# Kernel optimization log

Hardware: AMD Instinct MI355X
Metric: run time of the kernel (lower is better)

The kernel has to match this reference:

```python
import jax, jax.numpy as jnp
import numpy as np

MIN_SCALE = 0.2
MAX_SCALE = 1.0
RESIDUAL_WEIGHT = 0.7


def _conv(x, w, b, pad):
    # x: [B,Cin,H,W], w: [Cout,Cin,k,k]
    y = jax.lax.conv_general_dilated(
        x, w, window_strides=(1, 1), padding=[(pad, pad), (pad, pad)],
        dimension_numbers=("NCHW", "OIHW", "NCHW"))
    return y + b[None, :, None, None]


def setup_inputs() -> dict:
    key = jax.random.key(0)
    ks = jax.random.split(key, 12)
    B, C, H, W = 16, 64, 256, 256
    hidden = C // 2  # max(1, in_channels // 2)
    s = lambda fan_in: 1.0 / np.sqrt(fan_in)
    return {
        "x": jax.random.normal(ks[0], (B, C, H, W), jnp.float32),
        # per-kernel spatial attention convs (2 -> 1 channels)
        "w3": jax.random.normal(ks[1], (1, 2, 3, 3), jnp.float32) * s(2 * 9),
        "b3": jnp.zeros((1,), jnp.float32),
        "w5": jax.random.normal(ks[2], (1, 2, 5, 5), jnp.float32) * s(2 * 25),
        "b5": jnp.zeros((1,), jnp.float32),
        # fusion conv (len(kernel_sizes)=2 -> 1 channels, 1x1)
        "wf": jax.random.normal(ks[3], (1, 2, 1, 1), jnp.float32) * s(2),
        "bf": jnp.zeros((1,), jnp.float32),
        # channel_reduction: C -> 1, 1x1
        "wr": jax.random.normal(ks[4], (1, C, 1, 1), jnp.float32) * s(C),
        "br": jnp.zeros((1,), jnp.float32),
        # channel_attention MLP: 1 -> hidden -> C (1x1 convs)
        "wc1": jax.random.normal(ks[5], (hidden, 1, 1, 1), jnp.float32),
        "bc1": jnp.zeros((hidden,), jnp.float32),
        "wc2": jax.random.normal(ks[6], (C, hidden, 1, 1), jnp.float32) * s(hidden),
        "bc2": jnp.zeros((C,), jnp.float32),
    }


def reference(x, w3, b3, w5, b5, wf, bf, wr, br, wc1, bc1, wc2, bc2):
    # channel-pooled descriptor, shared across scales: [B,2,H,W]
    x_cat = jnp.concatenate(
        [jnp.mean(x, axis=1, keepdims=True), jnp.max(x, axis=1, keepdims=True)],
        axis=1)
    a3 = jax.nn.sigmoid(_conv(x_cat, w3, b3, 1))  # [B,1,H,W]
    a5 = jax.nn.sigmoid(_conv(x_cat, w5, b5, 2))  # [B,1,H,W]
    fused = _conv(jnp.concatenate([a3, a5], axis=1), wf, bf, 0)  # [B,1,H,W]
    # dropout is identity at inference
    fused = MIN_SCALE + (MAX_SCALE - MIN_SCALE) * fused
    spatial = x * fused  # [B,C,H,W]
    # channel attention: reduce channels -> global avg pool -> 1x1 MLP -> sigmoid
    reduced = _conv(spatial, wr, br, 0)                         # [B,1,H,W]
    pooled = jnp.mean(reduced, axis=(2, 3), keepdims=True)      # [B,1,1,1]
    h = jax.nn.relu(_conv(pooled, wc1, bc1, 0))                 # [B,hid,1,1]
    cw = jax.nn.sigmoid(_conv(h, wc2, bc2, 0))                  # [B,C,1,1]
    spatial = spatial * cw
    return spatial + RESIDUAL_WEIGHT * x
```

## Files before the change

kernel.cpp:

```cpp
#include <hip/hip_runtime.h>
#include <math.h>

#define BATCH 16
#define CH 64
#define HH 256
#define WW 256
#define HW (HH*WW)
#define HW4 (HW/4)
#define HIDDEN 32
#define GRP 4
#define NGRP (BATCH/GRP)
#define K2_BPB 256

typedef float nfloat4 __attribute__((ext_vector_type(4)));

__global__ __launch_bounds__(256) void msa_k1_reduce(
    const float* __restrict__ x, const float* __restrict__ wr,
    float* __restrict__ mm, float* __restrict__ xrp, int b0)
{
    __shared__ float part[3][64][13];
    int t = threadIdx.x;
    int p = t & 63;
    int q = t >> 6;
    int i4 = blockIdx.x * 64 + p;
    int bl = i4 >> 14;
    int p4 = i4 & (HW4 - 1);
    int b = b0 + bl;
    const float4* xb = (const float4*)x + (size_t)(b * CH + q * 16) * HW4 + p4;
    float sx = 0.f, sy = 0.f, sz = 0.f, sw = 0.f;
    float mx = -3.4e38f, my = -3.4e38f, mz = -3.4e38f, mw = -3.4e38f;
    float rx = 0.f, ry = 0.f, rz = 0.f, rw = 0.f;
    #pragma unroll 16
    for (int c = 0; c < 16; c++) {
        float4 v = xb[(size_t)c * HW4];
        float w = wr[q * 16 + c];
        sx += v.x; sy += v.y; sz += v.z; sw += v.w;
        mx = fmaxf(mx, v.x); my = fmaxf(my, v.y);
        mz = fmaxf(mz, v.z); mw = fmaxf(mw, v.w);
        rx += w * v.x; ry += w * v.y; rz += w * v.z; rw += w * v.w;
    }
    if (q) {
        float* d = part[q - 1][p];
        d[0] = sx; d[1] = sy; d[2] = sz; d[3] = sw;
        d[4] = mx; d[5] = my; d[6] = mz; d[7] = mw;
        d[8] = rx; d[9] = ry; d[10] = rz; d[11] = rw;
    }
    __syncthreads();
    if (q == 0) {
        #pragma unroll
        for (int k = 0; k < 3; k++) {
            const float* d = part[k][p];
            sx += d[0]; sy += d[1]; sz += d[2]; sw += d[3];
            mx = fmaxf(mx, d[4]); my = fmaxf(my, d[5]);
            mz = fmaxf(mz, d[6]); mw = fmaxf(mw, d[7]);
            rx += d[8]; ry += d[9]; rz += d[10]; rw += d[11];
        }
        const float inv = 1.0f / CH;
        size_t o = (size_t)b * HW4 + p4;
        float4 mm0 = {sx * inv, mx, sy * inv, my};
        float4 mm1 = {sz * inv, mz, sw * inv, mw};
        ((float4*)mm)[2 * o]     = mm0;
        ((float4*)mm)[2 * o + 1] = mm1;
        float4 xrv = {rx, ry, rz, rw};
        ((float4*)xrp)[o] = xrv;
    }
}

__global__ __launch_bounds__(256) void msa_k2_conv(
    const float* __restrict__ mm, const float* __restrict__ xrp,
    const float* __restrict__ w3, const float* __restrict__ b3,
    const float* __restrict__ w5, const float* __restrict__ b5,
    const float* __restrict__ wf, const float* __restrict__ bf,
    const float* __restrict__ br,
    const float* __restrict__ wc1, const float* __restrict__ bc1,
    const float* __restrict__ wc2, const float* __restrict__ bc2,
    float* __restrict__ fplane, float* __restrict__ sums,
    unsigned* __restrict__ cnt, float* __restrict__ cw, int b0)
{
    __shared__ float sm[2][20][20];
    __shared__ float wsum[4];
    __shared__ int lastflag;
    __shared__ float pooledS;
    __shared__ float hsh[HIDDEN];
    int b = b0 + blockIdx.z;
    int h0 = blockIdx.y * 16, w0 = blockIdx.x * 16;
    int tx = threadIdx.x, ty = threadIdx.y;
    int tid = ty * 16 + tx;
    const float2* mb = (const float2*)mm + (size_t)b * HW;
    for (int l = tid; l < 400; l += 256) {
        int lh = l / 20, lw = l % 20;
        int gh = h0 + lh - 2, gw = w0 + lw - 2;
        float vm = 0.f, vx = 0.f;
        if (gh >= 0 && gh < HH && gw >= 0 && gw < WW) {
            float2 v = mb[gh * WW + gw];
            vm = v.x; vx = v.y;
        }
        sm[0][lh][lw] = vm;
        sm[1][lh][lw] = vx;
    }
    __syncthreads();
    float s3 = b3[0];
    #pragma unroll
    for (int kh = 0; kh < 3; kh++)
        #pragma unroll
        for (int kw = 0; kw < 3; kw++)
            s3 += sm[0][ty + 1 + kh][tx + 1 + kw] * w3[kh * 3 + kw]
                + sm[1][ty + 1 + kh][tx + 1 + kw] * w3[9 + kh * 3 + kw];
    float s5 = b5[0];
    #pragma unroll
    for (int kh = 0; kh < 5; kh++)
        #pragma unroll
        for (int kw = 0; kw < 5; kw++)
            s5 += sm[0][ty + kh][tx + kw] * w5[kh * 5 + kw]
                + sm[1][ty + kh][tx + kw] * w5[25 + kh * 5 + kw];
    float a3 = 1.f / (1.f + expf(-s3));
    float a5 = 1.f / (1.f + expf(-s5));
    float fused = wf[0] * a3 + wf[1] * a5 + bf[0];
    float f = 0.2f + 0.8f * fused;
    int gh = h0 + ty, gw = w0 + tx;
    size_t po = (size_t)b * HW + gh * WW + gw;
    fplane[po] = f;
    float v = f * xrp[po];
    #pragma unroll
    for (int off = 32; off > 0; off >>= 1) v += __shfl_down(v, off);
    if ((tid & 63) == 0) wsum[tid >> 6] = v;
    __syncthreads();
    if (tid == 0) {
        float tot = wsum[0] + wsum[1] + wsum[2] + wsum[3];
        atomicAdd(&sums[b], tot);
        __threadfence();
        unsigned old = atomicAdd(&cnt[b], 1u);
        lastflag = (old == K2_BPB - 1) ? 1 : 0;
    }
    __syncthreads();
    if (lastflag) {
        if (tid == 0) {
            float tot = atomicAdd(&sums[b], 0.0f);
            pooledS = tot * (1.0f / HW) + br[0];
        }
        __syncthreads();
        if (tid < HIDDEN) hsh[tid] = fmaxf(wc1[tid] * pooledS + bc1[tid], 0.f);
        __syncthreads();
        if (tid < CH) {
            float acc = bc2[tid];
            #pragma unroll
            for (int j = 0; j < HIDDEN; j++) acc += wc2[tid * HIDDEN + j] * hsh[j];
            cw[b * CH + tid] = 1.f / (1.f + expf(-acc));
        }
    }
}

__global__ __launch_bounds__(256) void msa_k4_out(
    const float* __restrict__ x, const float* __restrict__ fplane,
    const float* __restrict__ cw, float* __restrict__ out, int b0)
{
    int idx = blockIdx.x * 256 + threadIdx.x;
    size_t base = (size_t)b0 * CH * HW4;
    int p = idx & (HW4 - 1);
    int bc = idx >> 14;
    int bl = bc >> 6;
    int b = b0 + bl;
    float s = cw[b * CH + (bc & 63)];
    float4 xv = ((const float4*)x)[base + idx];
    float4 fv = ((const float4*)fplane)[(size_t)b * HW4 + p];
    nfloat4 o;
    o.x = xv.x * (fv.x * s + 0.7f);
    o.y = xv.y * (fv.y * s + 0.7f);
    o.z = xv.z * (fv.z * s + 0.7f);
    o.w = xv.w * (fv.w * s + 0.7f);
    __builtin_nontemporal_store(o, ((nfloat4*)out) + base + idx);
}

extern "C" void kernel_launch(void* const* d_in, const int* in_sizes, int n_in,
                              void* d_out, int out_size, void* d_ws, size_t ws_size,
                              hipStream_t stream) {
    const float* x   = (const float*)d_in[0];
    const float* w3  = (const float*)d_in[1];
    const float* b3  = (const float*)d_in[2];
    const float* w5  = (const float*)d_in[3];
    const float* b5  = (const float*)d_in[4];
    const float* wf  = (const float*)d_in[5];
    const float* bf  = (const float*)d_in[6];
    const float* wr  = (const float*)d_in[7];
    const float* br  = (const float*)d_in[8];
    const float* wc1 = (const float*)d_in[9];
    const float* bc1 = (const float*)d_in[10];
    const float* wc2 = (const float*)d_in[11];
    const float* bc2 = (const float*)d_in[12];

    float* ws    = (float*)d_ws;
    float* mm    = ws;
    float* xrp   = ws + (size_t)2 * BATCH * HW;
    float* fpl   = ws + (size_t)3 * BATCH * HW;
    float* sums  = ws + (size_t)4 * BATCH * HW;
    unsigned* cnt = (unsigned*)(sums + BATCH);
    float* cw    = sums + 2 * BATCH;

    (void)hipMemsetAsync(sums, 0, 2 * BATCH * sizeof(float), stream);

    for (int g = 0; g < NGRP; ++g) {
        int b0 = g * GRP;
        msa_k1_reduce<<<GRP * HW4 / 64, 256, 0, stream>>>(x, wr, mm, xrp, b0);
        dim3 g2(WW / 16, HH / 16, GRP);
        msa_k2_conv<<<g2, dim3(16, 16), 0, stream>>>(mm, xrp, w3, b3, w5, b5,
                                                     wf, bf, br, wc1, bc1, wc2, bc2,
                                                     fpl, sums, cnt, cw, b0);
        msa_k4_out<<<GRP * CH * HW4 / 256, 256, 0, stream>>>(x, fpl, cw,
                                                             (float*)d_out, b0);
    }
}
```

Baseline: 620.1 us.

## Enlarge batch groups, drop split-channel reduction, reverse output block order

```diff
diff --git a/kernel.cpp b/kernel.cpp
--- a/kernel.cpp
+++ b/kernel.cpp
@@ -8,7 +8,7 @@
 #define HW (HH*WW)
 #define HW4 (HW/4)
 #define HIDDEN 32
-#define GRP 4
+#define GRP 8
 #define NGRP (BATCH/GRP)
 #define K2_BPB 256
 
@@ -16,54 +16,39 @@
 
 __global__ __launch_bounds__(256) void msa_k1_reduce(
     const float* __restrict__ x, const float* __restrict__ wr,
-    float* __restrict__ mm, float* __restrict__ xrp, int b0)
+    float* __restrict__ mm, float* __restrict__ xrp,
+    float* __restrict__ sums, unsigned* __restrict__ cnt, int b0)
 {
-    __shared__ float part[3][64][13];
-    int t = threadIdx.x;
-    int p = t & 63;
-    int q = t >> 6;
-    int i4 = blockIdx.x * 64 + p;
-    int bl = i4 >> 14;
-    int p4 = i4 & (HW4 - 1);
+    if (blockIdx.x == 0) {
+        int t = threadIdx.x;
+        if (t < GRP) sums[b0 + t] = 0.f;
+        else if (t < 2 * GRP) cnt[b0 + t - GRP] = 0u;
+    }
+    int idx = blockIdx.x * 256 + threadIdx.x;
+    int bl = idx >> 14;
+    int p4 = idx & (HW4 - 1);
     int b = b0 + bl;
-    const float4* xb = (const float4*)x + (size_t)(b * CH + q * 16) * HW4 + p4;
+    const float4* xb = (const float4*)x + (size_t)b * (CH * HW4) + p4;
     float sx = 0.f, sy = 0.f, sz = 0.f, sw = 0.f;
     float mx = -3.4e38f, my = -3.4e38f, mz = -3.4e38f, mw = -3.4e38f;
     float rx = 0.f, ry = 0.f, rz = 0.f, rw = 0.f;
-    #pragma unroll 16
-    for (int c = 0; c < 16; c++) {
+    #pragma unroll 8
+    for (int c = 0; c < CH; c++) {
         float4 v = xb[(size_t)c * HW4];
-        float w = wr[q * 16 + c];
+        float w = wr[c];
         sx += v.x; sy += v.y; sz += v.z; sw += v.w;
         mx = fmaxf(mx, v.x); my = fmaxf(my, v.y);
         mz = fmaxf(mz, v.z); mw = fmaxf(mw, v.w);
         rx += w * v.x; ry += w * v.y; rz += w * v.z; rw += w * v.w;
     }
-    if (q) {
-        float* d = part[q - 1][p];
-        d[0] = sx; d[1] = sy; d[2] = sz; d[3] = sw;
-        d[4] = mx; d[5] = my; d[6] = mz; d[7] = mw;
-        d[8] = rx; d[9] = ry; d[10] = rz; d[11] = rw;
-    }
-    __syncthreads();
-    if (q == 0) {
-        #pragma unroll
-        for (int k = 0; k < 3; k++) {
-            const float* d = part[k][p];
-            sx += d[0]; sy += d[1]; sz += d[2]; sw += d[3];
-            mx = fmaxf(mx, d[4]); my = fmaxf(my, d[5]);
-            mz = fmaxf(mz, d[6]); mw = fmaxf(mw, d[7]);
-            rx += d[8]; ry += d[9]; rz += d[10]; rw += d[11];
-        }
-        const float inv = 1.0f / CH;
-        size_t o = (size_t)b * HW4 + p4;
-        float4 mm0 = {sx * inv, mx, sy * inv, my};
-        float4 mm1 = {sz * inv, mz, sw * inv, mw};
-        ((float4*)mm)[2 * o]     = mm0;
-        ((float4*)mm)[2 * o + 1] = mm1;
-        float4 xrv = {rx, ry, rz, rw};
-        ((float4*)xrp)[o] = xrv;
-    }
+    const float inv = 1.0f / CH;
+    size_t o = (size_t)b * HW4 + p4;
+    float4 mm0 = {sx * inv, mx, sy * inv, my};
+    float4 mm1 = {sz * inv, mz, sw * inv, mw};
+    ((float4*)mm)[2 * o]     = mm0;
+    ((float4*)mm)[2 * o + 1] = mm1;
+    float4 xrv = {rx, ry, rz, rw};
+    ((float4*)xrp)[o] = xrv;
 }
 
 __global__ __launch_bounds__(256) void msa_k2_conv(
@@ -154,15 +139,15 @@
     const float* __restrict__ x, const float* __restrict__ fplane,
     const float* __restrict__ cw, float* __restrict__ out, int b0)
 {
-    int idx = blockIdx.x * 256 + threadIdx.x;
+    int bi = gridDim.x - 1 - blockIdx.x;
+    int idx = bi * 256 + threadIdx.x;
     size_t base = (size_t)b0 * CH * HW4;
-    int p = idx & (HW4 - 1);
+    int p  = idx & (HW4 - 1);
     int bc = idx >> 14;
-    int bl = bc >> 6;
-    int b = b0 + bl;
+    int b  = b0 + (bc >> 6);
     float s = cw[b * CH + (bc & 63)];
     float4 xv = ((const float4*)x)[base + idx];
-    float4 fv = ((const float4*)fplane)[(size_t)b * HW4 + p];
+    float4 fv = ((const float4*)fplane)[((size_t)b << 14) + p];
     nfloat4 o;
     o.x = xv.x * (fv.x * s + 0.7f);
     o.y = xv.y * (fv.y * s + 0.7f);
@@ -196,11 +181,10 @@
     unsigned* cnt = (unsigned*)(sums + BATCH);
     float* cw    = sums + 2 * BATCH;
 
-    (void)hipMemsetAsync(sums, 0, 2 * BATCH * sizeof(float), stream);
-
     for (int g = 0; g < NGRP; ++g) {
         int b0 = g * GRP;
-        msa_k1_reduce<<<GRP * HW4 / 64, 256, 0, stream>>>(x, wr, mm, xrp, b0);
+        msa_k1_reduce<<<GRP * HW4 / 256, 256, 0, stream>>>(x, wr, mm, xrp,
+                                                           sums, cnt, b0);
         dim3 g2(WW / 16, HH / 16, GRP);
         msa_k2_conv<<<g2, dim3(16, 16), 0, stream>>>(mm, xrp, w3, b3, w5, b5,
                                                      wf, bf, br, wc1, bc1, wc2, bc2,
```

After: 623.7 us. Within noise of the previous version (+0.6%).
